# Optimization experiments

Measured on AMD Instinct MI355X. Metric: run time of the kernel, lower is better.

## Reference

```python
import jax, jax.numpy as jnp
import numpy as np

N_EXPERTS = 16
TOP_K = 2
D_MODEL = 1024
D_FF = 1024
D_FF_SHARED = 2048
T_TOKENS = 4096


def setup_inputs() -> dict:
    key = jax.random.key(0)
    ks = jax.random.split(key, 7)
    s = 0.02
    return {
        "hidden_states": jax.random.normal(ks[0], (T_TOKENS, D_MODEL), jnp.float32),
        "gate_weight": jax.random.normal(ks[1], (N_EXPERTS, D_MODEL), jnp.float32) * s,
        "expert_gate_up": jax.random.normal(ks[2], (N_EXPERTS, 2 * D_FF, D_MODEL), jnp.float32) * s,
        "expert_down": jax.random.normal(ks[3], (N_EXPERTS, D_MODEL, D_FF), jnp.float32) * s,
        "shared_gate_up": jax.random.normal(ks[4], (2 * D_FF_SHARED, D_MODEL), jnp.float32) * s,
        "shared_down": jax.random.normal(ks[5], (D_MODEL, D_FF_SHARED), jnp.float32) * s,
        "shared_expert_gate_weight": jax.random.normal(ks[6], (1, D_MODEL), jnp.float32) * s,
    }


def _moe_forward(x, gate_weight, expert_gate_up, expert_down):
    T = x.shape[0]
    E = gate_weight.shape[0]
    # Router: top-k over logits, softmax over the selected logits (fp32)
    router_logits = x @ gate_weight.T                      # [T, E]
    topk_logits, topk_ids = jax.lax.top_k(router_logits, TOP_K)
    topk_weights = jax.nn.softmax(topk_logits.astype(jnp.float32), axis=-1)
    # Dense combine matrix C[t, e] = routing weight of expert e for token t
    combine = jnp.zeros((T, E), jnp.float32).at[
        jnp.arange(T)[:, None], topk_ids
    ].add(topk_weights)                                    # [T, E]

    # Scan over experts to avoid materializing [E, T, d]
    def body(acc, inputs):
        w_gu, w_d, c_e = inputs                            # [2F,d], [d,F], [T]
        gu = x @ w_gu.T                                    # [T, 2F]
        g, u = gu[:, :D_FF], gu[:, D_FF:]
        h = jax.nn.silu(g) * u                             # [T, F]
        acc = acc + c_e[:, None] * (h @ w_d.T)             # [T, d]
        return acc, None

    acc0 = jnp.zeros_like(x)
    moe_out, _ = jax.lax.scan(body, acc0, (expert_gate_up, expert_down, combine.T))
    return moe_out


def _shared_expert(x, shared_gate_up, shared_down, shared_expert_gate_weight):
    gu = x @ shared_gate_up.T                              # [T, 2Fs]
    mid = gu.shape[-1] // 2
    h = jax.nn.silu(gu[:, :mid]) * gu[:, mid:]
    out = h @ shared_down.T                                # [T, d]
    gate = jax.nn.sigmoid(x @ shared_expert_gate_weight.T)  # [T, 1]
    return out * gate


def reference(hidden_states, gate_weight, expert_gate_up, expert_down,
              shared_gate_up, shared_down, shared_expert_gate_weight):
    moe_out = _moe_forward(hidden_states, gate_weight, expert_gate_up, expert_down)
    shared_out = _shared_expert(hidden_states, shared_gate_up, shared_down,
                                shared_expert_gate_weight)
    return moe_out + shared_out
```

## Files before the change

kernel.cpp:

```cpp
#include <hip/hip_runtime.h>
#include <hip/hip_bf16.h>

#define T_TOKENS 4096
#define D_MODEL  1024
#define N_EXP    16
#define D_FF     1024
#define D_FF_SH  2048
#define MAX_T256 48

typedef __attribute__((ext_vector_type(8))) short short8;
typedef __attribute__((ext_vector_type(4))) float float4v;

__device__ __forceinline__ short f2bf(float f) {
    union { float f; unsigned u; } c; c.f = f;
    unsigned u = c.u + 0x7fffu + ((c.u >> 16) & 1u);
    return (short)(u >> 16);
}

__device__ __forceinline__ void gload16(const void* g, void* l) {
    __builtin_amdgcn_global_load_lds(
        (const __attribute__((address_space(1))) void*)g,
        (__attribute__((address_space(3))) void*)l, 16, 0, 0);
}

#define RING_TOP(VM) do { \
    asm volatile("s_waitcnt vmcnt(" #VM ") lgkmcnt(0)" ::: "memory"); \
    __builtin_amdgcn_s_barrier(); \
} while (0)

__global__ __launch_bounds__(256) void convert_all_kernel(
    const float* __restrict__ s0, short* __restrict__ d0,
    const float* __restrict__ s1, short* __restrict__ d1,
    const float* __restrict__ s2, short* __restrict__ d2,
    const float* __restrict__ s3, short* __restrict__ d3) {
    int c = blockIdx.x * 256 + threadIdx.x;
    const float* s; short* d; int off;
    if      (c < 4194304) { s = s0; d = d0; off = c; }
    else if (c < 6291456) { s = s1; d = d1; off = c - 4194304; }
    else if (c < 6815744) { s = s2; d = d2; off = c - 6291456; }
    else                  { s = s3; d = d3; off = c - 6815744; }
    size_t i = (size_t)off * 8;
    float4 a = *(const float4*)(s + i);
    float4 b = *(const float4*)(s + i + 4);
    union { short sh[8]; int4 v; } p;
    p.sh[0] = f2bf(a.x); p.sh[1] = f2bf(a.y); p.sh[2] = f2bf(a.z); p.sh[3] = f2bf(a.w);
    p.sh[4] = f2bf(b.x); p.sh[5] = f2bf(b.y); p.sh[6] = f2bf(b.z); p.sh[7] = f2bf(b.w);
    *(int4*)(d + i) = p.v;
}

__global__ __launch_bounds__(256) void router_kernel(
    const float* __restrict__ x, const float* __restrict__ gw, const float* __restrict__ sgw,
    short* __restrict__ xb, int* __restrict__ topk_id, float* __restrict__ topk_w,
    float* __restrict__ gate, int* __restrict__ counts) {
    __shared__ float gwl[17 * 1024];
    int tid = threadIdx.x;
#pragma unroll
    for (int i = 0; i < 16; i++)
        *(float4*)&gwl[tid * 4 + i * 1024] = *(const float4*)&gw[tid * 4 + i * 1024];
    *(float4*)&gwl[16384 + tid * 4] = *(const float4*)&sgw[tid * 4];
    __syncthreads();

    int wave = tid >> 6, lane = tid & 63;
    int t0 = blockIdx.x * 16 + wave * 4;

    float acc[4][17];
#pragma unroll
    for (int tt = 0; tt < 4; tt++)
#pragma unroll
        for (int e = 0; e < 17; e++) acc[tt][e] = 0.f;

#pragma unroll
    for (int i = 0; i < 4; i++) {
        int d = lane * 4 + i * 256;
        float4 xv[4];
#pragma unroll
        for (int tt = 0; tt < 4; tt++) {
            xv[tt] = *(const float4*)&x[(size_t)(t0 + tt) * D_MODEL + d];
            union { short sh[4]; int2 v; } p;
            p.sh[0] = f2bf(xv[tt].x); p.sh[1] = f2bf(xv[tt].y);
            p.sh[2] = f2bf(xv[tt].z); p.sh[3] = f2bf(xv[tt].w);
            *(int2*)&xb[(size_t)(t0 + tt) * D_MODEL + d] = p.v;
        }
#pragma unroll
        for (int e = 0; e < 17; e++) {
            float4 g = *(const float4*)&gwl[e * 1024 + d];
#pragma unroll
            for (int tt = 0; tt < 4; tt++)
                acc[tt][e] += xv[tt].x * g.x + xv[tt].y * g.y + xv[tt].z * g.z + xv[tt].w * g.w;
        }
    }

#pragma unroll
    for (int tt = 0; tt < 4; tt++)
#pragma unroll
        for (int e = 0; e < 17; e++)
            for (int off = 32; off; off >>= 1) acc[tt][e] += __shfl_xor(acc[tt][e], off);

    if (lane == 0) {
#pragma unroll
        for (int tt = 0; tt < 4; tt++) {
            int t = t0 + tt;
            float v1 = -1e30f, v2 = -1e30f; int i1 = 0, i2 = 0;
#pragma unroll
            for (int e = 0; e < 16; e++) {
                float v = acc[tt][e];
                if (v > v1) { v2 = v1; i2 = i1; v1 = v; i1 = e; }
                else if (v > v2) { v2 = v; i2 = e; }
            }
            float e2 = expf(v2 - v1);
            float s = 1.f + e2;
            topk_id[t * 2] = i1; topk_id[t * 2 + 1] = i2;
            topk_w[t * 2] = 1.f / s; topk_w[t * 2 + 1] = e2 / s;
            gate[t] = 1.f / (1.f + expf(-acc[tt][16]));
            atomicAdd(&counts[i1], 1); atomicAdd(&counts[i2], 1);
        }
    }
}

__global__ void offsets_kernel(const int* __restrict__ counts, int* __restrict__ offsets,
                               int* __restrict__ cursor, int* __restrict__ tile_map,
                               int* __restrict__ n_tiles) {
    if (threadIdx.x == 0) {
        int off = 0, nt = 0;
        for (int e = 0; e < N_EXP; e++) {
            offsets[e] = off; cursor[e] = off;
            int c = counts[e];
            for (int r = 0; r < c; r += 256) tile_map[nt++] = (e << 16) | (r >> 8);
            off += c;
        }
        n_tiles[0] = nt;
    }
}

__global__ __launch_bounds__(256) void scatter_kernel(
    const int* __restrict__ topk_id, const float* __restrict__ topk_w,
    int* __restrict__ cursor, int* __restrict__ tok_list, float* __restrict__ tok_w,
    int* __restrict__ slot_of) {
    int t = blockIdx.x * 256 + threadIdx.x;
#pragma unroll
    for (int k = 0; k < 2; k++) {
        int e = topk_id[t * 2 + k];
        int pos = atomicAdd(&cursor[e], 1);
        tok_list[pos] = t;
        tok_w[pos] = topk_w[t * 2 + k];
        slot_of[t * 2 + k] = pos;
    }
}

__global__ __launch_bounds__(512, 2) void gemm1_kernel(
    const short* __restrict__ xb,
    const short* __restrict__ Wexp,
    const short* __restrict__ Wsh,
    short* __restrict__ Hexp,
    short* __restrict__ Hsh,
    const int* __restrict__ tok_list,
    const int* __restrict__ offsets, const int* __restrict__ counts,
    const int* __restrict__ tile_map, const int* __restrict__ n_tiles) {
    int bx = blockIdx.x, by = blockIdx.y;
    int count, row0, dff;
    const int* idx = nullptr;
    const short* Wg; short* Hout;
    if (bx < MAX_T256) {
        if (by >= 8 || bx >= n_tiles[0]) return;
        int tm = tile_map[bx];
        int e = tm >> 16; row0 = (tm & 0xffff) << 8;
        count = counts[e];
        int base = offsets[e];
        idx = tok_list + base;
        Wg = Wexp + (size_t)e * 2 * D_FF * D_MODEL;
        Hout = Hexp + (size_t)base * D_FF;
        dff = D_FF;
    } else {
        row0 = (bx - MAX_T256) * 256; count = T_TOKENS;
        Wg = Wsh; Hout = Hsh; dff = D_FF_SH;
    }
    int col0 = by * 128;
    const short* Wu = Wg + (size_t)dff * D_MODEL;

    __shared__ char lds[131072];

    int t = threadIdx.x;
    int wave = t >> 6, lane = t & 63;
    int wm = (wave & 3) * 64, wn = (wave >> 2) * 64;
    int fr = lane & 15;
    int fk2p = ((((lane >> 4) + (fr >> 1)) & 3) << 4);

    float4v accg[4][4], accu[4][4];
#pragma unroll
    for (int i = 0; i < 4; i++)
#pragma unroll
        for (int j = 0; j < 4; j++) { accg[i][j] = (float4v)0.f; accu[i][j] = (float4v)0.f; }

    int rA = t >> 2;
    int csrc = ((t & 3) - (t >> 3)) & 3;
    int cq = csrc * 8;
    int r0c = min(row0 + rA, count - 1);
    int r1c = min(row0 + rA + 128, count - 1);
    int g0 = idx ? idx[r0c] : r0c;
    int g1 = idx ? idx[r1c] : r1c;
    const short* aP0 = xb + (size_t)g0 * D_MODEL + cq;
    const short* aP1 = xb + (size_t)g1 * D_MODEL + cq;
    const short* bgP = Wg + (size_t)(col0 + rA) * D_MODEL + cq;
    const short* buP = Wu + (size_t)(col0 + rA) * D_MODEL + cq;
    int lo = t * 16;

    auto stage = [&](int s) {
        char* base = lds + (s & 3) * 32768;
        int off = s * 32;
        gload16(aP0 + off, base + lo);
        gload16(aP1 + off, base + 8192 + lo);
        gload16(bgP + off, base + 16384 + lo);
        gload16(buP + off, base + 24576 + lo);
    };
    auto compute = [&](int k) {
        const char* sb = lds + (k & 3) * 32768;
        short8 af[4], bgf[4], buf4[4];
#pragma unroll
        for (int i = 0; i < 4; i++)
            af[i] = *(const short8*)(sb + (wm + i * 16 + fr) * 64 + fk2p);
#pragma unroll
        for (int j = 0; j < 4; j++) {
            bgf[j] = *(const short8*)(sb + 16384 + (wn + j * 16 + fr) * 64 + fk2p);
            buf4[j] = *(const short8*)(sb + 24576 + (wn + j * 16 + fr) * 64 + fk2p);
        }
        __builtin_amdgcn_s_setprio(1);
#pragma unroll
        for (int i = 0; i < 4; i++)
#pragma unroll
            for (int j = 0; j < 4; j++) {
                accg[i][j] = __builtin_amdgcn_mfma_f32_16x16x32_bf16(af[i], bgf[j], accg[i][j], 0, 0, 0);
                accu[i][j] = __builtin_amdgcn_mfma_f32_16x16x32_bf16(af[i], buf4[j], accu[i][j], 0, 0, 0);
            }
        __builtin_amdgcn_s_setprio(0);
    };

    const int NK = D_MODEL / 32;
    stage(0); stage(1); stage(2);
    int k = 0;
    for (; k < NK - 3; ++k) {
        RING_TOP(8);
        stage(k + 3);
        compute(k);
    }
    RING_TOP(8); compute(k); ++k;
    RING_TOP(4); compute(k); ++k;
    RING_TOP(0); compute(k);

    int erow = (lane >> 4) * 4;
    int ecol = lane & 15;
#pragma unroll
    for (int i = 0; i < 4; i++)
#pragma unroll
        for (int j = 0; j < 4; j++)
#pragma unroll
            for (int r = 0; r < 4; r++) {
                int row = wm + i * 16 + erow + r;
                if (row0 + row < count) {
                    float g = accg[i][j][r], u = accu[i][j][r];
                    float h = g / (1.f + expf(-g)) * u;
                    Hout[(size_t)(row0 + row) * dff + col0 + wn + j * 16 + ecol] = f2bf(h);
                }
            }
}

__global__ __launch_bounds__(512, 2) void gemm2_kernel(
    const short* __restrict__ Hexp, const short* __restrict__ Hsh,
    const short* __restrict__ Wdexp,
    const short* __restrict__ Wdsh,
    float* __restrict__ oslots,
    float* __restrict__ out,
    const float* __restrict__ tok_w, const float* __restrict__ gate,
    const int* __restrict__ offsets, const int* __restrict__ counts,
    const int* __restrict__ tile_map, const int* __restrict__ n_tiles) {
    int bx = blockIdx.x, by = blockIdx.y;
    int count, row0, K, base;
    const short* Ab; const short* B;
    bool shared_part;
    if (bx < MAX_T256) {
        if (bx >= n_tiles[0]) return;
        int tm = tile_map[bx];
        int e = tm >> 16; row0 = (tm & 0xffff) << 8;
        count = counts[e]; base = offsets[e];
        Ab = Hexp + (size_t)base * D_FF; K = D_FF;
        B = Wdexp + (size_t)e * D_MODEL * D_FF;
        shared_part = false;
    } else {
        row0 = (bx - MAX_T256) * 256; count = T_TOKENS; base = 0;
        Ab = Hsh; K = D_FF_SH; B = Wdsh; shared_part = true;
    }
    int col0 = by * 128;

    __shared__ char lds[147456];

    int t = threadIdx.x;
    int wave = t >> 6, lane = t & 63;
    int wm = (wave & 3) * 64, wn = (wave >> 2) * 64;
    int fr = lane & 15;
    int fk2p = ((((lane >> 4) + (fr >> 1)) & 3) << 4);

    float4v acc[4][4];
#pragma unroll
    for (int i = 0; i < 4; i++)
#pragma unroll
        for (int j = 0; j < 4; j++) acc[i][j] = (float4v)0.f;

    int rA = t >> 2;
    int csrc = ((t & 3) - (t >> 3)) & 3;
    int cq = csrc * 8;
    int r0c = min(row0 + rA, count - 1);
    int r1c = min(row0 + rA + 128, count - 1);
    const short* aP0 = Ab + (size_t)r0c * K + cq;
    const short* aP1 = Ab + (size_t)r1c * K + cq;
    const short* bP  = B + (size_t)(col0 + rA) * K + cq;
    int lo = t * 16;

    auto stage = [&](int pos, int s) {
        char* bb = lds + pos * 24576;
        int off = s * 32;
        gload16(aP0 + off, bb + lo);
        gload16(aP1 + off, bb + 8192 + lo);
        gload16(bP + off,  bb + 16384 + lo);
    };
    auto compute = [&](int pos) {
        const char* sb = lds + pos * 24576;
        short8 af[4], bf[4];
#pragma unroll
        for (int i = 0; i < 4; i++)
            af[i] = *(const short8*)(sb + (wm + i * 16 + fr) * 64 + fk2p);
#pragma unroll
        for (int j = 0; j < 4; j++)
            bf[j] = *(const short8*)(sb + 16384 + (wn + j * 16 + fr) * 64 + fk2p);
        __builtin_amdgcn_s_setprio(1);
#pragma unroll
        for (int i = 0; i < 4; i++)
#pragma unroll
            for (int j = 0; j < 4; j++)
                acc[i][j] = __builtin_amdgcn_mfma_f32_16x16x32_bf16(af[i], bf[j], acc[i][j], 0, 0, 0);
        __builtin_amdgcn_s_setprio(0);
    };

    const int NK = K / 32;
    stage(0, 0); stage(1, 1); stage(2, 2); stage(3, 3); stage(4, 4);
    int k = 0, spos = 5, cpos = 0;
    for (; k < NK - 5; ++k) {
        RING_TOP(12);
        stage(spos, k + 5); spos = (spos == 5) ? 0 : spos + 1;
        compute(cpos);      cpos = (cpos == 5) ? 0 : cpos + 1;
    }
    RING_TOP(12); compute(cpos); cpos = (cpos == 5) ? 0 : cpos + 1; ++k;
    RING_TOP(9);  compute(cpos); cpos = (cpos == 5) ? 0 : cpos + 1; ++k;
    RING_TOP(6);  compute(cpos); cpos = (cpos == 5) ? 0 : cpos + 1; ++k;
    RING_TOP(3);  compute(cpos); cpos = (cpos == 5) ? 0 : cpos + 1; ++k;
    RING_TOP(0);  compute(cpos);

    int erow = (lane >> 4) * 4;
    int ecol = lane & 15;
#pragma unroll
    for (int i = 0; i < 4; i++)
#pragma unroll
        for (int j = 0; j < 4; j++)
#pragma unroll
            for (int r = 0; r < 4; r++) {
                int row = wm + i * 16 + erow + r;
                if (row0 + row < count) {
                    float v = acc[i][j][r];
                    int col = col0 + wn + j * 16 + ecol;
                    if (!shared_part) {
                        int slot = base + row0 + row;
                        oslots[(size_t)slot * D_MODEL + col] = tok_w[slot] * v;
                    } else {
                        out[(size_t)(row0 + row) * D_MODEL + col] = gate[row0 + row] * v;
                    }
                }
            }
}

__global__ __launch_bounds__(256) void combine_kernel(
    float* __restrict__ out, const float* __restrict__ oslots,
    const int* __restrict__ slot_of) {
    int t = blockIdx.x;
    int sA = slot_of[t * 2], sB = slot_of[t * 2 + 1];
    int d = threadIdx.x * 4;
    float4 o = *(float4*)&out[(size_t)t * D_MODEL + d];
    float4 a = *(const float4*)&oslots[(size_t)sA * D_MODEL + d];
    float4 b = *(const float4*)&oslots[(size_t)sB * D_MODEL + d];
    o.x += a.x + b.x; o.y += a.y + b.y; o.z += a.z + b.z; o.w += a.w + b.w;
    *(float4*)&out[(size_t)t * D_MODEL + d] = o;
}

extern "C" void kernel_launch(void* const* d_in, const int* in_sizes, int n_in,
                              void* d_out, int out_size, void* d_ws, size_t ws_size,
                              hipStream_t stream) {
    const float* x     = (const float*)d_in[0];
    const float* gw    = (const float*)d_in[1];
    const float* egu   = (const float*)d_in[2];
    const float* edown = (const float*)d_in[3];
    const float* sgu   = (const float*)d_in[4];
    const float* sdown = (const float*)d_in[5];
    const float* sgate = (const float*)d_in[6];
    float* out = (float*)d_out;
    char* ws = (char*)d_ws;

    const size_t XB_OFF     = 0;
    const size_t WGU_OFF    = XB_OFF     + (size_t)4096*1024*2;
    const size_t WDOWN_OFF  = WGU_OFF    + (size_t)16*2048*1024*2;
    const size_t WSGU_OFF   = WDOWN_OFF  + (size_t)16*1024*1024*2;
    const size_t WSDOWN_OFF = WSGU_OFF   + (size_t)4096*1024*2;
    const size_t HEXP_OFF   = WSDOWN_OFF + (size_t)1024*2048*2;
    const size_t HSH_OFF    = HEXP_OFF   + (size_t)8192*1024*2;
    const size_t OSLOT_OFF  = HSH_OFF    + (size_t)4096*2048*2;
    const size_t TID_OFF    = OSLOT_OFF  + (size_t)8192*1024*4;
    const size_t TW_OFF     = TID_OFF    + 4096*2*4;
    const size_t GATE_OFF   = TW_OFF     + 4096*2*4;
    const size_t TOKL_OFF   = GATE_OFF   + 4096*4;
    const size_t TOKW_OFF   = TOKL_OFF   + 8192*4;
    const size_t SLOT_OFF   = TOKW_OFF   + 8192*4;
    const size_t CNT_OFF    = SLOT_OFF   + 8192*4;
    const size_t OFFS_OFF   = CNT_OFF    + 256;
    const size_t CUR_OFF    = OFFS_OFF   + 256;
    const size_t TMAP_OFF   = CUR_OFF    + 256;
    const size_t NT_OFF     = TMAP_OFF   + 512;

    short* xb      = (short*)(ws + XB_OFF);
    short* wgu_b   = (short*)(ws + WGU_OFF);
    short* wdown_b = (short*)(ws + WDOWN_OFF);
    short* wsgu_b  = (short*)(ws + WSGU_OFF);
    short* wsdn_b  = (short*)(ws + WSDOWN_OFF);
    short* h_exp   = (short*)(ws + HEXP_OFF);
    short* h_sh    = (short*)(ws + HSH_OFF);
    float* oslots  = (float*)(ws + OSLOT_OFF);
    int*   topk_id = (int*)(ws + TID_OFF);
    float* topk_w  = (float*)(ws + TW_OFF);
    float* gate    = (float*)(ws + GATE_OFF);
    int*   tok_l   = (int*)(ws + TOKL_OFF);
    float* tok_w   = (float*)(ws + TOKW_OFF);
    int*   slot_of = (int*)(ws + SLOT_OFF);
    int*   counts  = (int*)(ws + CNT_OFF);
    int*   offsets = (int*)(ws + OFFS_OFF);
    int*   cursor  = (int*)(ws + CUR_OFF);
    int*   tmap    = (int*)(ws + TMAP_OFF);
    int*   ntiles  = (int*)(ws + NT_OFF);

    hipMemsetAsync(counts, 0, 64, stream);

    convert_all_kernel<<<27648, 256, 0, stream>>>(egu, wgu_b, edown, wdown_b,
                                                  sgu, wsgu_b, sdown, wsdn_b);
    router_kernel<<<256, 256, 0, stream>>>(x, gw, sgate, xb, topk_id, topk_w, gate, counts);
    offsets_kernel<<<1, 64, 0, stream>>>(counts, offsets, cursor, tmap, ntiles);
    scatter_kernel<<<T_TOKENS / 256, 256, 0, stream>>>(topk_id, topk_w, cursor, tok_l, tok_w, slot_of);

    gemm1_kernel<<<dim3(MAX_T256 + 16, 16), 512, 0, stream>>>(
        xb, wgu_b, wsgu_b, h_exp, h_sh, tok_l, offsets, counts, tmap, ntiles);

    gemm2_kernel<<<dim3(MAX_T256 + 16, 8), 512, 0, stream>>>(
        h_exp, h_sh, wdown_b, wsdn_b, oslots, out, tok_w, gate, offsets, counts, tmap, ntiles);

    combine_kernel<<<T_TOKENS, 256, 0, stream>>>(out, oslots, slot_of);
}
```

Baseline: 606.5 us.

## Make expert GEMM kernels persistent with an atomic tile queue

Both GEMM kernels now launch a fixed 256 blocks that repeatedly claim tile ids from a global atomic counter until all tiles are done. Shared-expert tiles come first and routed-expert tiles follow, replacing the old 2D grid in which many blocks exited immediately for unused expert tiles. The counters are reset in the offsets kernel. The goal is to cut wasted block launches and even out the tail of the load. The cost is an atomic plus a block barrier per tile, and it assumes one resident block per CU is enough to keep the machine busy.

```diff
diff --git a/kernel.cpp b/kernel.cpp
--- a/kernel.cpp
+++ b/kernel.cpp
@@ -119,7 +119,7 @@
 
 __global__ void offsets_kernel(const int* __restrict__ counts, int* __restrict__ offsets,
                                int* __restrict__ cursor, int* __restrict__ tile_map,
-                               int* __restrict__ n_tiles) {
+                               int* __restrict__ n_tiles, int* __restrict__ gc) {
     if (threadIdx.x == 0) {
         int off = 0, nt = 0;
         for (int e = 0; e < N_EXP; e++) {
@@ -129,6 +129,7 @@
             off += c;
         }
         n_tiles[0] = nt;
+        gc[0] = 0; gc[1] = 0;
     }
 }
 
@@ -155,112 +156,123 @@
     short* __restrict__ Hsh,
     const int* __restrict__ tok_list,
     const int* __restrict__ offsets, const int* __restrict__ counts,
-    const int* __restrict__ tile_map, const int* __restrict__ n_tiles) {
-    int bx = blockIdx.x, by = blockIdx.y;
-    int count, row0, dff;
-    const int* idx = nullptr;
-    const short* Wg; short* Hout;
-    if (bx < MAX_T256) {
-        if (by >= 8 || bx >= n_tiles[0]) return;
-        int tm = tile_map[bx];
-        int e = tm >> 16; row0 = (tm & 0xffff) << 8;
-        count = counts[e];
-        int base = offsets[e];
-        idx = tok_list + base;
-        Wg = Wexp + (size_t)e * 2 * D_FF * D_MODEL;
-        Hout = Hexp + (size_t)base * D_FF;
-        dff = D_FF;
-    } else {
-        row0 = (bx - MAX_T256) * 256; count = T_TOKENS;
-        Wg = Wsh; Hout = Hsh; dff = D_FF_SH;
-    }
-    int col0 = by * 128;
-    const short* Wu = Wg + (size_t)dff * D_MODEL;
-
+    const int* __restrict__ tile_map, const int* __restrict__ n_tiles,
+    int* __restrict__ gc) {
     __shared__ char lds[131072];
+    __shared__ int s_tile;
 
     int t = threadIdx.x;
     int wave = t >> 6, lane = t & 63;
     int wm = (wave & 3) * 64, wn = (wave >> 2) * 64;
     int fr = lane & 15;
     int fk2p = ((((lane >> 4) + (fr >> 1)) & 3) << 4);
-
-    float4v accg[4][4], accu[4][4];
-#pragma unroll
-    for (int i = 0; i < 4; i++)
-#pragma unroll
-        for (int j = 0; j < 4; j++) { accg[i][j] = (float4v)0.f; accu[i][j] = (float4v)0.f; }
-
     int rA = t >> 2;
     int csrc = ((t & 3) - (t >> 3)) & 3;
     int cq = csrc * 8;
-    int r0c = min(row0 + rA, count - 1);
-    int r1c = min(row0 + rA + 128, count - 1);
-    int g0 = idx ? idx[r0c] : r0c;
-    int g1 = idx ? idx[r1c] : r1c;
-    const short* aP0 = xb + (size_t)g0 * D_MODEL + cq;
-    const short* aP1 = xb + (size_t)g1 * D_MODEL + cq;
-    const short* bgP = Wg + (size_t)(col0 + rA) * D_MODEL + cq;
-    const short* buP = Wu + (size_t)(col0 + rA) * D_MODEL + cq;
     int lo = t * 16;
 
-    auto stage = [&](int s) {
-        char* base = lds + (s & 3) * 32768;
-        int off = s * 32;
-        gload16(aP0 + off, base + lo);
-        gload16(aP1 + off, base + 8192 + lo);
-        gload16(bgP + off, base + 16384 + lo);
-        gload16(buP + off, base + 24576 + lo);
-    };
-    auto compute = [&](int k) {
-        const char* sb = lds + (k & 3) * 32768;
-        short8 af[4], bgf[4], buf4[4];
+    int nt = n_tiles[0];
+    int total = 256 + nt * 8;
+
+    for (;;) {
+        if (t == 0) s_tile = atomicAdd(gc, 1);
+        __syncthreads();
+        int id = s_tile;
+        if (id >= total) return;
+
+        int count, row0, dff, col0;
+        const int* idx = nullptr;
+        const short* Wg; short* Hout;
+        if (id < 256) {
+            row0 = (id >> 4) * 256; count = T_TOKENS;
+            Wg = Wsh; Hout = Hsh; dff = D_FF_SH; col0 = (id & 15) * 128;
+        } else {
+            int q = id - 256;
+            int tm = tile_map[q >> 3];
+            int e = tm >> 16; row0 = (tm & 0xffff) << 8;
+            count = counts[e];
+            int base = offsets[e];
+            idx = tok_list + base;
+            Wg = Wexp + (size_t)e * 2 * D_FF * D_MODEL;
+            Hout = Hexp + (size_t)base * D_FF;
+            dff = D_FF;
+            col0 = (q & 7) * 128;
+        }
+        const short* Wu = Wg + (size_t)dff * D_MODEL;
+
+        int r0c = min(row0 + rA, count - 1);
+        int r1c = min(row0 + rA + 128, count - 1);
+        int g0 = idx ? idx[r0c] : r0c;
+        int g1 = idx ? idx[r1c] : r1c;
+        const short* aP0 = xb + (size_t)g0 * D_MODEL + cq;
+        const short* aP1 = xb + (size_t)g1 * D_MODEL + cq;
+        const short* bgP = Wg + (size_t)(col0 + rA) * D_MODEL + cq;
+        const short* buP = Wu + (size_t)(col0 + rA) * D_MODEL + cq;
+
+        float4v accg[4][4], accu[4][4];
 #pragma unroll
         for (int i = 0; i < 4; i++)
-            af[i] = *(const short8*)(sb + (wm + i * 16 + fr) * 64 + fk2p);
-#pragma unroll
-        for (int j = 0; j < 4; j++) {
-            bgf[j] = *(const short8*)(sb + 16384 + (wn + j * 16 + fr) * 64 + fk2p);
-            buf4[j] = *(const short8*)(sb + 24576 + (wn + j * 16 + fr) * 64 + fk2p);
-        }
-        __builtin_amdgcn_s_setprio(1);
+#pragma unroll
+            for (int j = 0; j < 4; j++) { accg[i][j] = (float4v)0.f; accu[i][j] = (float4v)0.f; }
+
+        auto stage = [&](int s) {
+            char* base = lds + (s & 3) * 32768;
+            int off = s * 32;
+            gload16(aP0 + off, base + lo);
+            gload16(aP1 + off, base + 8192 + lo);
+            gload16(bgP + off, base + 16384 + lo);
+            gload16(buP + off, base + 24576 + lo);
+        };
+        auto compute = [&](int k) {
+            const char* sb = lds + (k & 3) * 32768;
+            short8 af[4], bgf[4], buf4[4];
+#pragma unroll
+            for (int i = 0; i < 4; i++)
+                af[i] = *(const short8*)(sb + (wm + i * 16 + fr) * 64 + fk2p);
+#pragma unroll
+            for (int j = 0; j < 4; j++) {
+                bgf[j] = *(const short8*)(sb + 16384 + (wn + j * 16 + fr) * 64 + fk2p);
+                buf4[j] = *(const short8*)(sb + 24576 + (wn + j * 16 + fr) * 64 + fk2p);
+            }
+            __builtin_amdgcn_s_setprio(1);
+#pragma unroll
+            for (int i = 0; i < 4; i++)
+#pragma unroll
+                for (int j = 0; j < 4; j++) {
+                    accg[i][j] = __builtin_amdgcn_mfma_f32_16x16x32_bf16(af[i], bgf[j], accg[i][j], 0, 0, 0);
+                    accu[i][j] = __builtin_amdgcn_mfma_f32_16x16x32_bf16(af[i], buf4[j], accu[i][j], 0, 0, 0);
+                }
+            __builtin_amdgcn_s_setprio(0);
+        };
+
+        const int NK = D_MODEL / 32;
+        stage(0); stage(1); stage(2);
+        int k = 0;
+        for (; k < NK - 3; ++k) {
+            RING_TOP(8);
+            stage(k + 3);
+            compute(k);
+        }
+        RING_TOP(8); compute(k); ++k;
+        RING_TOP(4); compute(k); ++k;
+        RING_TOP(0); compute(k);
+
+        int erow = (lane >> 4) * 4;
+        int ecol = lane & 15;
 #pragma unroll
         for (int i = 0; i < 4; i++)
 #pragma unroll
-            for (int j = 0; j < 4; j++) {
-                accg[i][j] = __builtin_amdgcn_mfma_f32_16x16x32_bf16(af[i], bgf[j], accg[i][j], 0, 0, 0);
-                accu[i][j] = __builtin_amdgcn_mfma_f32_16x16x32_bf16(af[i], buf4[j], accu[i][j], 0, 0, 0);
-            }
-        __builtin_amdgcn_s_setprio(0);
-    };
-
-    const int NK = D_MODEL / 32;
-    stage(0); stage(1); stage(2);
-    int k = 0;
-    for (; k < NK - 3; ++k) {
-        RING_TOP(8);
-        stage(k + 3);
-        compute(k);
-    }
-    RING_TOP(8); compute(k); ++k;
-    RING_TOP(4); compute(k); ++k;
-    RING_TOP(0); compute(k);
-
-    int erow = (lane >> 4) * 4;
-    int ecol = lane & 15;
-#pragma unroll
-    for (int i = 0; i < 4; i++)
-#pragma unroll
-        for (int j = 0; j < 4; j++)
-#pragma unroll
-            for (int r = 0; r < 4; r++) {
-                int row = wm + i * 16 + erow + r;
-                if (row0 + row < count) {
-                    float g = accg[i][j][r], u = accu[i][j][r];
-                    float h = g / (1.f + expf(-g)) * u;
-                    Hout[(size_t)(row0 + row) * dff + col0 + wn + j * 16 + ecol] = f2bf(h);
+            for (int j = 0; j < 4; j++)
+#pragma unroll
+                for (int r = 0; r < 4; r++) {
+                    int row = wm + i * 16 + erow + r;
+                    if (row0 + row < count) {
+                        float g = accg[i][j][r], u = accu[i][j][r];
+                        float h = g / (1.f + expf(-g)) * u;
+                        Hout[(size_t)(row0 + row) * dff + col0 + wn + j * 16 + ecol] = f2bf(h);
+                    }
                 }
-            }
+    }
 }
 
 __global__ __launch_bounds__(512, 2) void gemm2_kernel(
@@ -271,108 +283,120 @@
     float* __restrict__ out,
     const float* __restrict__ tok_w, const float* __restrict__ gate,
     const int* __restrict__ offsets, const int* __restrict__ counts,
-    const int* __restrict__ tile_map, const int* __restrict__ n_tiles) {
-    int bx = blockIdx.x, by = blockIdx.y;
-    int count, row0, K, base;
-    const short* Ab; const short* B;
-    bool shared_part;
-    if (bx < MAX_T256) {
-        if (bx >= n_tiles[0]) return;
-        int tm = tile_map[bx];
-        int e = tm >> 16; row0 = (tm & 0xffff) << 8;
-        count = counts[e]; base = offsets[e];
-        Ab = Hexp + (size_t)base * D_FF; K = D_FF;
-        B = Wdexp + (size_t)e * D_MODEL * D_FF;
-        shared_part = false;
-    } else {
-        row0 = (bx - MAX_T256) * 256; count = T_TOKENS; base = 0;
-        Ab = Hsh; K = D_FF_SH; B = Wdsh; shared_part = true;
-    }
-    int col0 = by * 128;
-
+    const int* __restrict__ tile_map, const int* __restrict__ n_tiles,
+    int* __restrict__ gc) {
     __shared__ char lds[147456];
+    __shared__ int s_tile;
 
     int t = threadIdx.x;
     int wave = t >> 6, lane = t & 63;
     int wm = (wave & 3) * 64, wn = (wave >> 2) * 64;
     int fr = lane & 15;
     int fk2p = ((((lane >> 4) + (fr >> 1)) & 3) << 4);
-
-    float4v acc[4][4];
-#pragma unroll
-    for (int i = 0; i < 4; i++)
-#pragma unroll
-        for (int j = 0; j < 4; j++) acc[i][j] = (float4v)0.f;
-
     int rA = t >> 2;
     int csrc = ((t & 3) - (t >> 3)) & 3;
     int cq = csrc * 8;
-    int r0c = min(row0 + rA, count - 1);
-    int r1c = min(row0 + rA + 128, count - 1);
-    const short* aP0 = Ab + (size_t)r0c * K + cq;
-    const short* aP1 = Ab + (size_t)r1c * K + cq;
-    const short* bP  = B + (size_t)(col0 + rA) * K + cq;
     int lo = t * 16;
 
-    auto stage = [&](int pos, int s) {
-        char* bb = lds + pos * 24576;
-        int off = s * 32;
-        gload16(aP0 + off, bb + lo);
-        gload16(aP1 + off, bb + 8192 + lo);
-        gload16(bP + off,  bb + 16384 + lo);
-    };
-    auto compute = [&](int pos) {
-        const char* sb = lds + pos * 24576;
-        short8 af[4], bf[4];
+    int nt = n_tiles[0];
+    int total = 128 + nt * 8;
+
+    for (;;) {
+        if (t == 0) s_tile = atomicAdd(gc, 1);
+        __syncthreads();
+        int id = s_tile;
+        if (id >= total) return;
+
+        int count, row0, K, base, col0;
+        const short* Ab; const short* B;
+        bool shared_part;
+        if (id < 128) {
+            row0 = (id >> 3) * 256; count = T_TOKENS; base = 0;
+            Ab = Hsh; K = D_FF_SH; B = Wdsh; shared_part = true;
+            col0 = (id & 7) * 128;
+        } else {
+            int q = id - 128;
+            int tm = tile_map[q >> 3];
+            int e = tm >> 16; row0 = (tm & 0xffff) << 8;
+            count = counts[e]; base = offsets[e];
+            Ab = Hexp + (size_t)base * D_FF; K = D_FF;
+            B = Wdexp + (size_t)e * D_MODEL * D_FF;
+            shared_part = false;
+            col0 = (q & 7) * 128;
+        }
+
+        int r0c = min(row0 + rA, count - 1);
+        int r1c = min(row0 + rA + 128, count - 1);
+        const short* aP0 = Ab + (size_t)r0c * K + cq;
+        const short* aP1 = Ab + (size_t)r1c * K + cq;
+        const short* bP  = B + (size_t)(col0 + rA) * K + cq;
+
+        float4v acc[4][4];
 #pragma unroll
         for (int i = 0; i < 4; i++)
-            af[i] = *(const short8*)(sb + (wm + i * 16 + fr) * 64 + fk2p);
-#pragma unroll
-        for (int j = 0; j < 4; j++)
-            bf[j] = *(const short8*)(sb + 16384 + (wn + j * 16 + fr) * 64 + fk2p);
-        __builtin_amdgcn_s_setprio(1);
+#pragma unroll
+            for (int j = 0; j < 4; j++) acc[i][j] = (float4v)0.f;
+
+        auto stage = [&](int pos, int s) {
+            char* bb = lds + pos * 24576;
+            int off = s * 32;
+            gload16(aP0 + off, bb + lo);
+            gload16(aP1 + off, bb + 8192 + lo);
+            gload16(bP + off,  bb + 16384 + lo);
+        };
+        auto compute = [&](int pos) {
+            const char* sb = lds + pos * 24576;
+            short8 af[4], bf[4];
+#pragma unroll
+            for (int i = 0; i < 4; i++)
+                af[i] = *(const short8*)(sb + (wm + i * 16 + fr) * 64 + fk2p);
+#pragma unroll
+            for (int j = 0; j < 4; j++)
+                bf[j] = *(const short8*)(sb + 16384 + (wn + j * 16 + fr) * 64 + fk2p);
+            __builtin_amdgcn_s_setprio(1);
+#pragma unroll
+            for (int i = 0; i < 4; i++)
+#pragma unroll
+                for (int j = 0; j < 4; j++)
+                    acc[i][j] = __builtin_amdgcn_mfma_f32_16x16x32_bf16(af[i], bf[j], acc[i][j], 0, 0, 0);
+            __builtin_amdgcn_s_setprio(0);
+        };
+
+        const int NK = K / 32;
+        stage(0, 0); stage(1, 1); stage(2, 2); stage(3, 3); stage(4, 4);
+        int k = 0, spos = 5, cpos = 0;
+        for (; k < NK - 5; ++k) {
+            RING_TOP(12);
+            stage(spos, k + 5); spos = (spos == 5) ? 0 : spos + 1;
+            compute(cpos);      cpos = (cpos == 5) ? 0 : cpos + 1;
+        }
+        RING_TOP(12); compute(cpos); cpos = (cpos == 5) ? 0 : cpos + 1; ++k;
+        RING_TOP(9);  compute(cpos); cpos = (cpos == 5) ? 0 : cpos + 1; ++k;
+        RING_TOP(6);  compute(cpos); cpos = (cpos == 5) ? 0 : cpos + 1; ++k;
+        RING_TOP(3);  compute(cpos); cpos = (cpos == 5) ? 0 : cpos + 1; ++k;
+        RING_TOP(0);  compute(cpos);
+
+        int erow = (lane >> 4) * 4;
+        int ecol = lane & 15;
 #pragma unroll
         for (int i = 0; i < 4; i++)
 #pragma unroll
             for (int j = 0; j < 4; j++)
-                acc[i][j] = __builtin_amdgcn_mfma_f32_16x16x32_bf16(af[i], bf[j], acc[i][j], 0, 0, 0);
-        __builtin_amdgcn_s_setprio(0);
-    };
-
-    const int NK = K / 32;
-    stage(0, 0); stage(1, 1); stage(2, 2); stage(3, 3); stage(4, 4);
-    int k = 0, spos = 5, cpos = 0;
-    for (; k < NK - 5; ++k) {
-        RING_TOP(12);
-        stage(spos, k + 5); spos = (spos == 5) ? 0 : spos + 1;
-        compute(cpos);      cpos = (cpos == 5) ? 0 : cpos + 1;
-    }
-    RING_TOP(12); compute(cpos); cpos = (cpos == 5) ? 0 : cpos + 1; ++k;
-    RING_TOP(9);  compute(cpos); cpos = (cpos == 5) ? 0 : cpos + 1; ++k;
-    RING_TOP(6);  compute(cpos); cpos = (cpos == 5) ? 0 : cpos + 1; ++k;
-    RING_TOP(3);  compute(cpos); cpos = (cpos == 5) ? 0 : cpos + 1; ++k;
-    RING_TOP(0);  compute(cpos);
-
-    int erow = (lane >> 4) * 4;
-    int ecol = lane & 15;
-#pragma unroll
-    for (int i = 0; i < 4; i++)
-#pragma unroll
-        for (int j = 0; j < 4; j++)
-#pragma unroll
-            for (int r = 0; r < 4; r++) {
-                int row = wm + i * 16 + erow + r;
-                if (row0 + row < count) {
-                    float v = acc[i][j][r];
-                    int col = col0 + wn + j * 16 + ecol;
-                    if (!shared_part) {
-                        int slot = base + row0 + row;
-                        oslots[(size_t)slot * D_MODEL + col] = tok_w[slot] * v;
-                    } else {
-                        out[(size_t)(row0 + row) * D_MODEL + col] = gate[row0 + row] * v;
+#pragma unroll
+                for (int r = 0; r < 4; r++) {
+                    int row = wm + i * 16 + erow + r;
+                    if (row0 + row < count) {
+                        float v = acc[i][j][r];
+                        int col = col0 + wn + j * 16 + ecol;
+                        if (!shared_part) {
+                            int slot = base + row0 + row;
+                            oslots[(size_t)slot * D_MODEL + col] = tok_w[slot] * v;
+                        } else {
+                            out[(size_t)(row0 + row) * D_MODEL + col] = gate[row0 + row] * v;
+                        }
                     }
                 }
-            }
+    }
 }
 
 __global__ __launch_bounds__(256) void combine_kernel(
@@ -420,6 +444,7 @@
     const size_t CUR_OFF    = OFFS_OFF   + 256;
     const size_t TMAP_OFF   = CUR_OFF    + 256;
     const size_t NT_OFF     = TMAP_OFF   + 512;
+    const size_t GC_OFF     = NT_OFF     + 16;
 
     short* xb      = (short*)(ws + XB_OFF);
     short* wgu_b   = (short*)(ws + WGU_OFF);
@@ -440,20 +465,21 @@
     int*   cursor  = (int*)(ws + CUR_OFF);
     int*   tmap    = (int*)(ws + TMAP_OFF);
     int*   ntiles  = (int*)(ws + NT_OFF);
+    int*   gcnt    = (int*)(ws + GC_OFF);
 
     hipMemsetAsync(counts, 0, 64, stream);
 
     convert_all_kernel<<<27648, 256, 0, stream>>>(egu, wgu_b, edown, wdown_b,
                                                   sgu, wsgu_b, sdown, wsdn_b);
     router_kernel<<<256, 256, 0, stream>>>(x, gw, sgate, xb, topk_id, topk_w, gate, counts);
-    offsets_kernel<<<1, 64, 0, stream>>>(counts, offsets, cursor, tmap, ntiles);
+    offsets_kernel<<<1, 64, 0, stream>>>(counts, offsets, cursor, tmap, ntiles, gcnt);
     scatter_kernel<<<T_TOKENS / 256, 256, 0, stream>>>(topk_id, topk_w, cursor, tok_l, tok_w, slot_of);
 
-    gemm1_kernel<<<dim3(MAX_T256 + 16, 16), 512, 0, stream>>>(
-        xb, wgu_b, wsgu_b, h_exp, h_sh, tok_l, offsets, counts, tmap, ntiles);
-
-    gemm2_kernel<<<dim3(MAX_T256 + 16, 8), 512, 0, stream>>>(
-        h_exp, h_sh, wdown_b, wsdn_b, oslots, out, tok_w, gate, offsets, counts, tmap, ntiles);
+    gemm1_kernel<<<256, 512, 0, stream>>>(
+        xb, wgu_b, wsgu_b, h_exp, h_sh, tok_l, offsets, counts, tmap, ntiles, gcnt);
+
+    gemm2_kernel<<<256, 512, 0, stream>>>(
+        h_exp, h_sh, wdown_b, wsdn_b, oslots, out, tok_w, gate, offsets, counts, tmap, ntiles, gcnt + 1);
 
     combine_kernel<<<T_TOKENS, 256, 0, stream>>>(out, oslots, slot_of);
 }
```

New measurement: 647.7 us. +6.8%, slower.

## Split gemm1 K-step into gate/up phases, reshape grids, shrink gemm2 ring for occupancy

Applied to the files above, without the earlier changes.

gemm1 now splits each K-step into two phases, one for the gate MFMAs and one for the up MFMAs. Prefetch loads are interleaved between the phases, with explicit s_barrier and sched_barrier. The gemm1 grid is reshaped so the shared-expert tiles use 8 y-blocks with a linearized id, which removes the idle by>=8 expert blocks. gemm2 cuts its LDS ring from 6 stages to 3 (72KB) and raises launch bounds to 4 blocks per CU, trading pipeline depth for occupancy. It also places the shared-expert tiles first in the grid and trims the grid to the maximum expert tile count.

```diff
diff --git a/kernel.cpp b/kernel.cpp
--- a/kernel.cpp
+++ b/kernel.cpp
@@ -26,6 +26,11 @@
 #define RING_TOP(VM) do { \
     asm volatile("s_waitcnt vmcnt(" #VM ") lgkmcnt(0)" ::: "memory"); \
     __builtin_amdgcn_s_barrier(); \
+} while (0)
+
+#define PHASE_BAR() do { \
+    asm volatile("s_barrier" ::: "memory"); \
+    __builtin_amdgcn_sched_barrier(0); \
 } while (0)
 
 __global__ __launch_bounds__(256) void convert_all_kernel(
@@ -157,11 +162,11 @@
     const int* __restrict__ offsets, const int* __restrict__ counts,
     const int* __restrict__ tile_map, const int* __restrict__ n_tiles) {
     int bx = blockIdx.x, by = blockIdx.y;
-    int count, row0, dff;
+    int count, row0, dff, col0;
     const int* idx = nullptr;
     const short* Wg; short* Hout;
     if (bx < MAX_T256) {
-        if (by >= 8 || bx >= n_tiles[0]) return;
+        if (bx >= n_tiles[0]) return;
         int tm = tile_map[bx];
         int e = tm >> 16; row0 = (tm & 0xffff) << 8;
         count = counts[e];
@@ -170,11 +175,13 @@
         Wg = Wexp + (size_t)e * 2 * D_FF * D_MODEL;
         Hout = Hexp + (size_t)base * D_FF;
         dff = D_FF;
+        col0 = by * 128;
     } else {
-        row0 = (bx - MAX_T256) * 256; count = T_TOKENS;
+        int id = (bx - MAX_T256) * 8 + by;
+        row0 = (id >> 4) * 256; count = T_TOKENS;
         Wg = Wsh; Hout = Hsh; dff = D_FF_SH;
-    }
-    int col0 = by * 128;
+        col0 = (id & 15) * 128;
+    }
     const short* Wu = Wg + (size_t)dff * D_MODEL;
 
     __shared__ char lds[131072];
@@ -184,16 +191,11 @@
     int wm = (wave & 3) * 64, wn = (wave >> 2) * 64;
     int fr = lane & 15;
     int fk2p = ((((lane >> 4) + (fr >> 1)) & 3) << 4);
-
-    float4v accg[4][4], accu[4][4];
-#pragma unroll
-    for (int i = 0; i < 4; i++)
-#pragma unroll
-        for (int j = 0; j < 4; j++) { accg[i][j] = (float4v)0.f; accu[i][j] = (float4v)0.f; }
-
     int rA = t >> 2;
     int csrc = ((t & 3) - (t >> 3)) & 3;
     int cq = csrc * 8;
+    int lo = t * 16;
+
     int r0c = min(row0 + rA, count - 1);
     int r1c = min(row0 + rA + 128, count - 1);
     int g0 = idx ? idx[r0c] : r0c;
@@ -202,7 +204,12 @@
     const short* aP1 = xb + (size_t)g1 * D_MODEL + cq;
     const short* bgP = Wg + (size_t)(col0 + rA) * D_MODEL + cq;
     const short* buP = Wu + (size_t)(col0 + rA) * D_MODEL + cq;
-    int lo = t * 16;
+
+    float4v accg[4][4], accu[4][4];
+#pragma unroll
+    for (int i = 0; i < 4; i++)
+#pragma unroll
+        for (int j = 0; j < 4; j++) { accg[i][j] = (float4v)0.f; accu[i][j] = (float4v)0.f; }
 
     auto stage = [&](int s) {
         char* base = lds + (s & 3) * 32768;
@@ -212,39 +219,49 @@
         gload16(bgP + off, base + 16384 + lo);
         gload16(buP + off, base + 24576 + lo);
     };
-    auto compute = [&](int k) {
+
+    auto step = [&](int k, bool pf) {
         const char* sb = lds + (k & 3) * 32768;
-        short8 af[4], bgf[4], buf4[4];
+        char* nb = lds + ((k + 3) & 3) * 32768;
+        int off3 = (k + 3) * 32;
+        if (pf) { gload16(aP0 + off3, nb + lo); gload16(aP1 + off3, nb + 8192 + lo); }
+        short8 af[4], bgf[4];
 #pragma unroll
         for (int i = 0; i < 4; i++)
             af[i] = *(const short8*)(sb + (wm + i * 16 + fr) * 64 + fk2p);
 #pragma unroll
-        for (int j = 0; j < 4; j++) {
+        for (int j = 0; j < 4; j++)
             bgf[j] = *(const short8*)(sb + 16384 + (wn + j * 16 + fr) * 64 + fk2p);
+        PHASE_BAR();
+        __builtin_amdgcn_s_setprio(1);
+#pragma unroll
+        for (int i = 0; i < 4; i++)
+#pragma unroll
+            for (int j = 0; j < 4; j++)
+                accg[i][j] = __builtin_amdgcn_mfma_f32_16x16x32_bf16(af[i], bgf[j], accg[i][j], 0, 0, 0);
+        __builtin_amdgcn_s_setprio(0);
+        if (pf) { gload16(bgP + off3, nb + 16384 + lo); gload16(buP + off3, nb + 24576 + lo); }
+        short8 buf4[4];
+#pragma unroll
+        for (int j = 0; j < 4; j++)
             buf4[j] = *(const short8*)(sb + 24576 + (wn + j * 16 + fr) * 64 + fk2p);
-        }
+        PHASE_BAR();
         __builtin_amdgcn_s_setprio(1);
 #pragma unroll
         for (int i = 0; i < 4; i++)
 #pragma unroll
-            for (int j = 0; j < 4; j++) {
-                accg[i][j] = __builtin_amdgcn_mfma_f32_16x16x32_bf16(af[i], bgf[j], accg[i][j], 0, 0, 0);
+            for (int j = 0; j < 4; j++)
                 accu[i][j] = __builtin_amdgcn_mfma_f32_16x16x32_bf16(af[i], buf4[j], accu[i][j], 0, 0, 0);
-            }
         __builtin_amdgcn_s_setprio(0);
     };
 
     const int NK = D_MODEL / 32;
     stage(0); stage(1); stage(2);
     int k = 0;
-    for (; k < NK - 3; ++k) {
-        RING_TOP(8);
-        stage(k + 3);
-        compute(k);
-    }
-    RING_TOP(8); compute(k); ++k;
-    RING_TOP(4); compute(k); ++k;
-    RING_TOP(0); compute(k);
+    for (; k < NK - 3; ++k) { RING_TOP(8); step(k, true); }
+    RING_TOP(8); step(k, false); ++k;
+    RING_TOP(4); step(k, false); ++k;
+    RING_TOP(0); step(k, false);
 
     int erow = (lane >> 4) * 4;
     int ecol = lane & 15;
@@ -263,7 +280,7 @@
             }
 }
 
-__global__ __launch_bounds__(512, 2) void gemm2_kernel(
+__global__ __launch_bounds__(512, 4) void gemm2_kernel(
     const short* __restrict__ Hexp, const short* __restrict__ Hsh,
     const short* __restrict__ Wdexp,
     const short* __restrict__ Wdsh,
@@ -273,46 +290,49 @@
     const int* __restrict__ offsets, const int* __restrict__ counts,
     const int* __restrict__ tile_map, const int* __restrict__ n_tiles) {
     int bx = blockIdx.x, by = blockIdx.y;
-    int count, row0, K, base;
+    int count, row0, K, base, col0;
     const short* Ab; const short* B;
     bool shared_part;
-    if (bx < MAX_T256) {
-        if (bx >= n_tiles[0]) return;
-        int tm = tile_map[bx];
+    if (bx < 16) {
+        int id = bx * 8 + by;
+        row0 = (id >> 3) * 256; count = T_TOKENS; base = 0;
+        Ab = Hsh; K = D_FF_SH; B = Wdsh; shared_part = true;
+        col0 = (id & 7) * 128;
+    } else {
+        int q = bx - 16;
+        if (q >= n_tiles[0]) return;
+        int tm = tile_map[q];
         int e = tm >> 16; row0 = (tm & 0xffff) << 8;
         count = counts[e]; base = offsets[e];
         Ab = Hexp + (size_t)base * D_FF; K = D_FF;
         B = Wdexp + (size_t)e * D_MODEL * D_FF;
         shared_part = false;
-    } else {
-        row0 = (bx - MAX_T256) * 256; count = T_TOKENS; base = 0;
-        Ab = Hsh; K = D_FF_SH; B = Wdsh; shared_part = true;
-    }
-    int col0 = by * 128;
-
-    __shared__ char lds[147456];
+        col0 = by * 128;
+    }
+
+    __shared__ char lds[73728];
 
     int t = threadIdx.x;
     int wave = t >> 6, lane = t & 63;
     int wm = (wave & 3) * 64, wn = (wave >> 2) * 64;
     int fr = lane & 15;
     int fk2p = ((((lane >> 4) + (fr >> 1)) & 3) << 4);
-
-    float4v acc[4][4];
-#pragma unroll
-    for (int i = 0; i < 4; i++)
-#pragma unroll
-        for (int j = 0; j < 4; j++) acc[i][j] = (float4v)0.f;
-
     int rA = t >> 2;
     int csrc = ((t & 3) - (t >> 3)) & 3;
     int cq = csrc * 8;
+    int lo = t * 16;
+
     int r0c = min(row0 + rA, count - 1);
     int r1c = min(row0 + rA + 128, count - 1);
     const short* aP0 = Ab + (size_t)r0c * K + cq;
     const short* aP1 = Ab + (size_t)r1c * K + cq;
     const short* bP  = B + (size_t)(col0 + rA) * K + cq;
-    int lo = t * 16;
+
+    float4v acc[4][4];
+#pragma unroll
+    for (int i = 0; i < 4; i++)
+#pragma unroll
+        for (int j = 0; j < 4; j++) acc[i][j] = (float4v)0.f;
 
     auto stage = [&](int pos, int s) {
         char* bb = lds + pos * 24576;
@@ -340,18 +360,15 @@
     };
 
     const int NK = K / 32;
-    stage(0, 0); stage(1, 1); stage(2, 2); stage(3, 3); stage(4, 4);
-    int k = 0, spos = 5, cpos = 0;
-    for (; k < NK - 5; ++k) {
-        RING_TOP(12);
-        stage(spos, k + 5); spos = (spos == 5) ? 0 : spos + 1;
-        compute(cpos);      cpos = (cpos == 5) ? 0 : cpos + 1;
-    }
-    RING_TOP(12); compute(cpos); cpos = (cpos == 5) ? 0 : cpos + 1; ++k;
-    RING_TOP(9);  compute(cpos); cpos = (cpos == 5) ? 0 : cpos + 1; ++k;
-    RING_TOP(6);  compute(cpos); cpos = (cpos == 5) ? 0 : cpos + 1; ++k;
-    RING_TOP(3);  compute(cpos); cpos = (cpos == 5) ? 0 : cpos + 1; ++k;
-    RING_TOP(0);  compute(cpos);
+    stage(0, 0); stage(1, 1);
+    int k = 0, spos = 2, cpos = 0;
+    for (; k < NK - 2; ++k) {
+        RING_TOP(3);
+        stage(spos, k + 2); spos = (spos == 2) ? 0 : spos + 1;
+        compute(cpos);      cpos = (cpos == 2) ? 0 : cpos + 1;
+    }
+    RING_TOP(3); compute(cpos); cpos = (cpos == 2) ? 0 : cpos + 1; ++k;
+    RING_TOP(0); compute(cpos);
 
     int erow = (lane >> 4) * 4;
     int ecol = lane & 15;
@@ -449,10 +466,10 @@
     offsets_kernel<<<1, 64, 0, stream>>>(counts, offsets, cursor, tmap, ntiles);
     scatter_kernel<<<T_TOKENS / 256, 256, 0, stream>>>(topk_id, topk_w, cursor, tok_l, tok_w, slot_of);
 
-    gemm1_kernel<<<dim3(MAX_T256 + 16, 16), 512, 0, stream>>>(
+    gemm1_kernel<<<dim3(MAX_T256 + 32, 8), 512, 0, stream>>>(
         xb, wgu_b, wsgu_b, h_exp, h_sh, tok_l, offsets, counts, tmap, ntiles);
 
-    gemm2_kernel<<<dim3(MAX_T256 + 16, 8), 512, 0, stream>>>(
+    gemm2_kernel<<<dim3(64, 8), 512, 0, stream>>>(
         h_exp, h_sh, wdown_b, wsdn_b, oslots, out, tok_w, gate, offsets, counts, tmap, ntiles);
 
     combine_kernel<<<T_TOKENS, 256, 0, stream>>>(out, oslots, slot_of);
```

Result: faster. 593.0 us (-2.2%).
